# Kernel tuning notes

Measured on AMD Instinct MI355X. Metric: run time of the kernel, lower is better.

The kernel has to match this reference:

```python
import jax, jax.numpy as jnp
import numpy as np

N = 60000    # total nodes
E = 600000   # total edges
R = 7        # num relations (edge types)
D_IN = 64    # raw node feature dim
D = 128      # hidden_channels
D2 = 64      # hidden_channels // 2
L = 2        # num_layers
EPS = 1e-5   # LayerNorm eps (torch default)


def setup_inputs() -> dict:
    key = jax.random.key(0)
    ks = jax.random.split(key, 10)
    s = 0.05  # xavier-ish scale
    return {
        "x": jax.random.normal(ks[0], (N, D_IN), jnp.float32),
        "edge_index": jax.random.randint(ks[1], (2, E), 0, N, dtype=jnp.int64),
        "edge_type": jax.random.randint(ks[2], (E,), 0, R, dtype=jnp.int64),
        "emb_W": jax.random.normal(ks[3], (D_IN, D), jnp.float32) * s,
        "emb_b": jnp.zeros((D,), jnp.float32),
        "rel_W": jax.random.normal(ks[4], (L, R, D, D), jnp.float32) * s,
        "root_W": jax.random.normal(ks[5], (L, D, D), jnp.float32) * s,
        "conv_b": jnp.zeros((L, D), jnp.float32),
        "ln_g": jnp.ones((L, D), jnp.float32),
        "ln_b": jnp.zeros((L, D), jnp.float32),
        "cls_W1": jax.random.normal(ks[6], (D, D2), jnp.float32) * s,
        "cls_b1": jnp.zeros((D2,), jnp.float32),
        "cls_ln_g": jnp.ones((D2,), jnp.float32),
        "cls_ln_b": jnp.zeros((D2,), jnp.float32),
        "cls_W2": jax.random.normal(ks[7], (D2, 1), jnp.float32) * s,
        "cls_b2": jnp.zeros((1,), jnp.float32),
    }


def _layernorm(h, g, b):
    m = h.mean(-1, keepdims=True)
    v = h.var(-1, keepdims=True)  # population variance, matches torch LayerNorm
    return (h - m) * jax.lax.rsqrt(v + EPS) * g + b


def _rgcn_conv(h, Wrel, Wroot, b, src, dst, edge_type):
    # Transform every node by every relation weight: [R*N, D]
    t = jnp.einsum('nd,rde->rne', h, Wrel).reshape(R * N, D)
    msg = t[edge_type * N + src]                      # [E, D] per-edge messages
    seg = edge_type * N + dst                         # per-(relation, dst) segments
    summed = jax.ops.segment_sum(msg, seg, num_segments=R * N)
    cnt = jax.ops.segment_sum(jnp.ones((E,), msg.dtype), seg, num_segments=R * N)
    mean = summed / jnp.maximum(cnt, 1.0)[:, None]    # scatter-mean per relation
    agg = mean.reshape(R, N, D).sum(0)                # sum over relations
    return agg + h @ Wroot + b


def reference(x, edge_index, edge_type, emb_W, emb_b, rel_W, root_W, conv_b,
              ln_g, ln_b, cls_W1, cls_b1, cls_ln_g, cls_ln_b, cls_W2, cls_b2):
    src, dst = edge_index[0], edge_index[1]
    # Node embedding (features clamped as in original forward)
    h = jnp.clip(x, -10.0, 10.0) @ emb_W + emb_b
    for l in range(L):
        h = _rgcn_conv(h, rel_W[l], root_W[l], conv_b[l], src, dst, edge_type)
        h = jax.nn.relu(_layernorm(h, ln_g[l], ln_b[l]))
        # dropout is identity at inference
    # Classifier on transaction nodes (= all nodes in this unified setup)
    z = jax.nn.relu(_layernorm(h @ cls_W1 + cls_b1, cls_ln_g, cls_ln_b))
    return z @ cls_W2 + cls_b2  # [N, 1] logits
```

## Files before the change

### kernel.cpp

```cpp
#include <hip/hip_runtime.h>
#include <hip/hip_bf16.h>

typedef unsigned int uint;
typedef unsigned short ushort;

#define N_NODES 60000
#define N_EDGES 600000
#define NREL 7
#define D_IN 64
#define DHID 128
#define LEPS 1e-5f
#define EMB_BLKS 938

typedef __attribute__((ext_vector_type(8))) short bf16x8v;
typedef __attribute__((ext_vector_type(4))) float f32x4v;

#define AS1C(p) ((const __attribute__((address_space(1))) void*)(p))
#define AS3(p)  ((__attribute__((address_space(3))) void*)(p))

__device__ __forceinline__ float bf2f(uint u16) {
    return __uint_as_float(u16 << 16);
}
__device__ __forceinline__ uint f2bf(float f) {
    uint u = __float_as_uint(f);
    uint lsb = (u >> 16) & 1u;
    u += 0x7fffu + lsb;
    return u >> 16;
}
__device__ __forceinline__ uint pack2(float a, float b) {
    return f2bf(a) | (f2bf(b) << 16);
}

__global__ __launch_bounds__(256) void k_prep(const float* __restrict__ relW,
                                              const float* __restrict__ rootW,
                                              const float* __restrict__ embW,
                                              const int* __restrict__ dst,
                                              const int* __restrict__ et,
                                              ushort* __restrict__ Btr,
                                              ushort* __restrict__ Bte,
                                              int* __restrict__ deg8) {
    __shared__ float t[64][65];
    const int tid = threadIdx.x;
    if (blockIdx.x < 64) {
        const int l  = blockIdx.x >> 5;
        const int b5 = blockIdx.x & 31;
        const int r  = b5 >> 2;
        const int kt = (b5 >> 1) & 1;
        const int jt = b5 & 1;
        #pragma unroll
        for (int i = 0; i < 4; ++i) {
            const int idx = i * 256 + tid;
            const int kr = idx >> 4;
            const int j4 = idx & 15;
            const int kg = kt * 64 + kr;
            const float* src = (r < 7)
                ? (relW + (((size_t)l * 7 + r) * 128 + kg) * 128 + jt * 64 + j4 * 4)
                : (rootW + ((size_t)l * 128 + kg) * 128 + jt * 64 + j4 * 4);
            const float4 v = *(const float4*)src;
            t[kr][j4 * 4 + 0] = v.x; t[kr][j4 * 4 + 1] = v.y;
            t[kr][j4 * 4 + 2] = v.z; t[kr][j4 * 4 + 3] = v.w;
        }
        __syncthreads();
        uint* btd = (uint*)Btr;
        #pragma unroll
        for (int i = 0; i < 8; ++i) {
            const int idx = i * 256 + tid;
            const int jr = idx >> 5;
            const int kd = idx & 31;
            const uint w = pack2(t[kd * 2][jr], t[kd * 2 + 1][jr]);
            btd[((size_t)(l * 8 + r) * 128 + jt * 64 + jr) * 64 + kt * 32 + kd] = w;
        }
    } else if (blockIdx.x < 66) {
        const int jt = blockIdx.x - 64;
        #pragma unroll
        for (int i = 0; i < 4; ++i) {
            const int idx = i * 256 + tid;
            const int kr = idx >> 4;
            const int j4 = idx & 15;
            const float4 v = *(const float4*)(embW + (size_t)kr * 128 + jt * 64 + j4 * 4);
            t[kr][j4 * 4 + 0] = v.x; t[kr][j4 * 4 + 1] = v.y;
            t[kr][j4 * 4 + 2] = v.z; t[kr][j4 * 4 + 3] = v.w;
        }
        __syncthreads();
        uint* btd = (uint*)Bte;
        #pragma unroll
        for (int i = 0; i < 8; ++i) {
            const int idx = i * 256 + tid;
            const int jr = idx >> 5;
            const int kd = idx & 31;
            const uint w = pack2(t[kd * 2][jr], t[kd * 2 + 1][jr]);
            btd[(size_t)(jt * 64 + jr) * 32 + kd] = w;
        }
    } else {
        for (int e = (blockIdx.x - 66) * 256 + tid; e < N_EDGES; e += 1024 * 256)
            atomicAdd(&deg8[dst[e] * 8 + et[e]], 1);
    }
}

__global__ void k_scan1n(const int* __restrict__ deg8, int* __restrict__ rp,
                         int* __restrict__ bsum, int n) {
    __shared__ int s[256];
    const int t = threadIdx.x;
    const int i = blockIdx.x * 256 + t;
    int v = 0;
    if (i < n) {
        const int4 x = *(const int4*)(deg8 + (size_t)i * 8);
        const int4 y = *(const int4*)(deg8 + (size_t)i * 8 + 4);
        v = x.x + x.y + x.z + x.w + y.x + y.y + y.z + y.w;
    }
    s[t] = v;
    __syncthreads();
    for (int o = 1; o < 256; o <<= 1) {
        int uu = (t >= o) ? s[t - o] : 0;
        __syncthreads();
        s[t] += uu;
        __syncthreads();
    }
    if (i < n) rp[i] = s[t] - v;
    if (t == 255) bsum[blockIdx.x] = s[255];
}
__global__ void k_scanmid(int* __restrict__ bs, int nb) {
    __shared__ int s[256];
    __shared__ int carrys;
    const int t = threadIdx.x;
    if (t == 0) carrys = 0;
    __syncthreads();
    const int nch = (nb + 255) / 256;
    for (int ch = 0; ch < nch; ++ch) {
        const int i = ch * 256 + t;
        const int v = (i < nb) ? bs[i] : 0;
        s[t] = v;
        __syncthreads();
        for (int o = 1; o < 256; o <<= 1) {
            int uu = (t >= o) ? s[t - o] : 0;
            __syncthreads();
            s[t] += uu;
            __syncthreads();
        }
        const int carry = carrys;
        if (i < nb) bs[i] = s[t] - v + carry;
        __syncthreads();
        if (t == 255) carrys = carry + s[255];
        __syncthreads();
    }
}
__global__ void k_scanadd(int* __restrict__ a, const int* __restrict__ bsums,
                          int* __restrict__ fill, int n) {
    const int i = blockIdx.x * 256 + threadIdx.x;
    if (i < n) {
        const int v = a[i] + bsums[blockIdx.x];
        a[i] = v;
        fill[i] = v;
    }
    if (blockIdx.x == 0 && threadIdx.x == 0) a[n] = N_EDGES;
}

__global__ __launch_bounds__(256) void k_scatemb(const float* __restrict__ x,
                                                 const ushort* __restrict__ Bte,
                                                 const float* __restrict__ ebias,
                                                 ushort* __restrict__ h,
                                                 const int* __restrict__ src,
                                                 const int* __restrict__ dst,
                                                 const int* __restrict__ et,
                                                 int* __restrict__ fill,
                                                 uint* __restrict__ csr32) {
    __shared__ alignas(16) ushort sa[64 * 64];
    __shared__ alignas(16) ushort sb[128 * 64];
    const int tid = threadIdx.x;
    if (blockIdx.x >= EMB_BLKS) {
        for (int e = (blockIdx.x - EMB_BLKS) * 256 + tid; e < N_EDGES; e += 1024 * 256) {
            const int d = dst[e];
            const int r = et[e];
            const int p = atomicAdd(&fill[d], 1);
            csr32[p] = ((uint)r << 20) | (uint)(r * N_NODES + src[e]);
        }
        return;
    }
    const int lane = tid & 63;
    const int wid = tid >> 6;
    const int wrow = wid >> 1, wcol = wid & 1;
    const int l15 = lane & 15, lh = lane >> 4;
    const int row0 = blockIdx.x * 64;

    #pragma unroll
    for (int i = 0; i < 2; ++i) {
        const int p = i * 256 + tid;
        const int row = p >> 3, gq = p & 7;
        const int n = min(row0 + row, N_NODES - 1);
        const float4 xa = *(const float4*)(x + (size_t)n * 64 + gq * 8);
        const float4 xb = *(const float4*)(x + (size_t)n * 64 + gq * 8 + 4);
        uint w[4];
        w[0] = pack2(fminf(fmaxf(xa.x, -10.f), 10.f), fminf(fmaxf(xa.y, -10.f), 10.f));
        w[1] = pack2(fminf(fmaxf(xa.z, -10.f), 10.f), fminf(fmaxf(xa.w, -10.f), 10.f));
        w[2] = pack2(fminf(fmaxf(xb.x, -10.f), 10.f), fminf(fmaxf(xb.y, -10.f), 10.f));
        w[3] = pack2(fminf(fmaxf(xb.z, -10.f), 10.f), fminf(fmaxf(xb.w, -10.f), 10.f));
        *(uint4*)&sa[(row * 8 + (gq ^ (row & 7))) * 8] = make_uint4(w[0], w[1], w[2], w[3]);
    }
    #pragma unroll
    for (int i = 0; i < 4; ++i) {
        const int p = i * 256 + tid;
        const int row = p >> 3, gq = p & 7;
        const uint4 v = *(const uint4*)((const uint*)Bte + (size_t)row * 32 + gq * 4);
        *(uint4*)&sb[(row * 8 + (gq ^ (row & 7))) * 8] = v;
    }
    float bv[4];
    #pragma unroll
    for (int fn = 0; fn < 4; ++fn) bv[fn] = ebias[wcol * 64 + fn * 16 + l15];
    __syncthreads();

    f32x4v acc[2][4];
    #pragma unroll
    for (int fm = 0; fm < 2; ++fm)
        #pragma unroll
        for (int fn = 0; fn < 4; ++fn)
            acc[fm][fn] = (f32x4v){0.f, 0.f, 0.f, 0.f};
    #pragma unroll
    for (int kh = 0; kh < 2; ++kh) {
        bf16x8v af[2], bfr[4];
        #pragma unroll
        for (int fm = 0; fm < 2; ++fm) {
            const int rowa = wrow * 32 + fm * 16 + l15;
            const int slot = (kh * 4 + lh) ^ (rowa & 7);
            af[fm] = *(const bf16x8v*)&sa[rowa * 64 + slot * 8];
        }
        #pragma unroll
        for (int fn = 0; fn < 4; ++fn) {
            const int rowb = wcol * 64 + fn * 16 + l15;
            const int slot = (kh * 4 + lh) ^ (rowb & 7);
            bfr[fn] = *(const bf16x8v*)&sb[rowb * 64 + slot * 8];
        }
        #pragma unroll
        for (int fm = 0; fm < 2; ++fm)
            #pragma unroll
            for (int fn = 0; fn < 4; ++fn)
                acc[fm][fn] = __builtin_amdgcn_mfma_f32_16x16x32_bf16(
                    af[fm], bfr[fn], acc[fm][fn], 0, 0, 0);
    }
    #pragma unroll
    for (int fm = 0; fm < 2; ++fm)
        #pragma unroll
        for (int r = 0; r < 4; ++r) {
            const int row = row0 + wrow * 32 + fm * 16 + lh * 4 + r;
            if (row < N_NODES) {
                #pragma unroll
                for (int fn = 0; fn < 4; ++fn) {
                    const int col = wcol * 64 + fn * 16 + l15;
                    h[(size_t)row * 128 + col] = (ushort)f2bf(acc[fm][fn][r] + bv[fn]);
                }
            }
        }
}

__global__ __launch_bounds__(512) void k_trans(const ushort* __restrict__ h16,
                                               const ushort* __restrict__ Btr,
                                               ushort* __restrict__ T16,
                                               int nrows) {
    __shared__ alignas(16) ushort sa[2][8192];
    __shared__ alignas(16) ushort sb[2][8192];
    const int tid = threadIdx.x;
    const int lane = tid & 63;
    const int wid = tid >> 6;
    const int wrow = wid >> 1, wcol = wid & 1;
    const int l15 = lane & 15, lh = lane >> 4;
    const int row0 = blockIdx.x * 128;
    const int bj = blockIdx.y;

    int prow[2], pG[2], arow[2];
    #pragma unroll
    for (int hf = 0; hf < 2; ++hf) {
        const int p = hf * 512 + wid * 64 + lane;
        const int r = p >> 3;
        prow[hf] = r;
        pG[hf] = (p & 7) ^ (r & 7);
        arow[hf] = min(row0 + r, nrows - 1);
    }
    #pragma unroll
    for (int kt = 0; kt < 2; ++kt) {
        #pragma unroll
        for (int hf = 0; hf < 2; ++hf) {
            const ushort* ga = h16 + (size_t)arow[hf] * 128 + kt * 64 + pG[hf] * 8;
            __builtin_amdgcn_global_load_lds(AS1C(ga),
                AS3(&sa[kt][(hf * 512 + wid * 64) * 8]), 16, 0, 0);
            const ushort* gb = Btr + ((size_t)bj * 128 + prow[hf]) * 128 + kt * 64 + pG[hf] * 8;
            __builtin_amdgcn_global_load_lds(AS1C(gb),
                AS3(&sb[kt][(hf * 512 + wid * 64) * 8]), 16, 0, 0);
        }
    }
    __syncthreads();

    f32x4v acc[2][4];
    #pragma unroll
    for (int fm = 0; fm < 2; ++fm)
        #pragma unroll
        for (int fn = 0; fn < 4; ++fn)
            acc[fm][fn] = (f32x4v){0.f, 0.f, 0.f, 0.f};

    #pragma unroll
    for (int kt = 0; kt < 2; ++kt)
        #pragma unroll
        for (int kh = 0; kh < 2; ++kh) {
            bf16x8v af[2], bfr[4];
            #pragma unroll
            for (int fm = 0; fm < 2; ++fm) {
                const int rowa = wrow * 32 + fm * 16 + l15;
                const int slot = (kh * 4 + lh) ^ (rowa & 7);
                af[fm] = *(const bf16x8v*)&sa[kt][rowa * 64 + slot * 8];
            }
            #pragma unroll
            for (int fn = 0; fn < 4; ++fn) {
                const int rowb = wcol * 64 + fn * 16 + l15;
                const int slot = (kh * 4 + lh) ^ (rowb & 7);
                bfr[fn] = *(const bf16x8v*)&sb[kt][rowb * 64 + slot * 8];
            }
            #pragma unroll
            for (int fm = 0; fm < 2; ++fm)
                #pragma unroll
                for (int fn = 0; fn < 4; ++fn)
                    acc[fm][fn] = __builtin_amdgcn_mfma_f32_16x16x32_bf16(
                        af[fm], bfr[fn], acc[fm][fn], 0, 0, 0);
        }

    #pragma unroll
    for (int fm = 0; fm < 2; ++fm)
        #pragma unroll
        for (int r = 0; r < 4; ++r) {
            const int row = row0 + wrow * 32 + fm * 16 + lh * 4 + r;
            if (row < nrows) {
                ushort* tp = T16 + ((size_t)bj * N_NODES + row) * 128 + wcol * 64 + l15;
                #pragma unroll
                for (int fn = 0; fn < 4; ++fn)
                    tp[fn * 16] = (ushort)f2bf(acc[fm][fn][r]);
            }
        }
}

__global__ __launch_bounds__(256) void k_gather(const uint* __restrict__ T32,
                                                const int* __restrict__ rp,
                                                const int* __restrict__ deg8,
                                                const uint* __restrict__ csr32,
                                                const float* __restrict__ bias,
                                                const float* __restrict__ g,
                                                const float* __restrict__ bb,
                                                uint* __restrict__ hout) {
    __shared__ float sinv[4][8];
    const int wave = (blockIdx.x * 256 + threadIdx.x) >> 6;
    const int lane = threadIdx.x & 63;
    const int wid = (threadIdx.x >> 6) & 3;
    const int nwaves = gridDim.x * 4;
    const float2 bias2 = *(const float2*)(bias + 2 * lane);
    const float2 g2 = *(const float2*)(g + 2 * lane);
    const float2 b2 = *(const float2*)(bb + 2 * lane);
    #pragma unroll 1
    for (int n0 = wave; n0 < N_NODES; n0 += nwaves) {
        const int n = __builtin_amdgcn_readfirstlane(n0);
        const int beg = __builtin_amdgcn_readfirstlane(rp[n]);
        const int end = __builtin_amdgcn_readfirstlane(rp[n + 1]);
        if (lane < 8) {
            const int c = deg8[(size_t)n * 8 + lane];
            sinv[wid][lane] = 1.0f / (float)max(c, 1);
        }
        float ax = 0.f, ay = 0.f;
        #pragma unroll 1
        for (int e = beg; e < end; e += 8) {
            const int4 c0 = *(const int4*)(csr32 + e);
            const int4 c1 = *(const int4*)(csr32 + e + 4);
            int t[8] = {c0.x, c0.y, c0.z, c0.w, c1.x, c1.y, c1.z, c1.w};
            #pragma unroll
            for (int q = 0; q < 8; ++q) t[q] = __builtin_amdgcn_readfirstlane(t[q]);
            uint v[8];
            #pragma unroll
            for (int q = 0; q < 8; ++q)
                if (e + q < end) v[q] = T32[(size_t)(t[q] & 0xFFFFF) * 64 + lane];
            #pragma unroll
            for (int q = 0; q < 8; ++q)
                if (e + q < end) {
                    const float w = sinv[wid][(t[q] >> 20) & 7];
                    ax += w * __uint_as_float(v[q] << 16);
                    ay += w * __uint_as_float(v[q] & 0xFFFF0000u);
                }
        }
        const uint vr = T32[((size_t)7 * N_NODES + n) * 64 + lane];
        const float c0f = ax + bf2f(vr & 0xFFFFu) + bias2.x;
        const float c1f = ay + bf2f(vr >> 16) + bias2.y;
        float s = c0f + c1f, sq = c0f * c0f + c1f * c1f;
        #pragma unroll
        for (int o = 1; o < 64; o <<= 1) {
            s += __shfl_xor(s, o, 64);
            sq += __shfl_xor(sq, o, 64);
        }
        const float mean = s * (1.f / 128.f);
        const float var = sq * (1.f / 128.f) - mean * mean;
        const float rs = rsqrtf(var + LEPS);
        const float y0 = fmaxf((c0f - mean) * rs * g2.x + b2.x, 0.f);
        const float y1 = fmaxf((c1f - mean) * rs * g2.y + b2.y, 0.f);
        hout[(size_t)n * 64 + lane] = pack2(y0, y1);
    }
}

__global__ __launch_bounds__(256) void k_cls(const ushort* __restrict__ h16,
                                             const float* __restrict__ W1,
                                             const float* __restrict__ b1,
                                             const float* __restrict__ lg,
                                             const float* __restrict__ lb,
                                             const float* __restrict__ W2,
                                             const float* __restrict__ b2,
                                             float* __restrict__ outp, int nrows) {
    __shared__ ushort Bs[16 * 64 * 8];
    const int tid = threadIdx.x;
    #pragma unroll
    for (int i = 0; i < 8; ++i) {
        const int q = i * 256 + tid;
        const int k = q >> 4;
        const int j0 = (q & 15) * 4;
        const float4 w = *(const float4*)(W1 + (size_t)k * 64 + j0);
        const int gg = k >> 3, kp = k & 7;
        const int jx = (gg & 3) << 4;
        Bs[(gg * 64 + ((j0 + 0) ^ jx)) * 8 + kp] = (ushort)f2bf(w.x);
        Bs[(gg * 64 + ((j0 + 1) ^ jx)) * 8 + kp] = (ushort)f2bf(w.y);
        Bs[(gg * 64 + ((j0 + 2) ^ jx)) * 8 + kp] = (ushort)f2bf(w.z);
        Bs[(gg * 64 + ((j0 + 3) ^ jx)) * 8 + kp] = (ushort)f2bf(w.w);
    }
    const int lane = tid & 63, wid = tid >> 6;
    const int l15 = lane & 15, lh = lane >> 4;
    float lgv[4], lbv[4], w2v[4], b1v[4];
    #pragma unroll
    for (int fn = 0; fn < 4; ++fn) {
        const int col = fn * 16 + l15;
        lgv[fn] = lg[col]; lbv[fn] = lb[col]; w2v[fn] = W2[col]; b1v[fn] = b1[col];
    }
    const float b2v = b2[0];
    __syncthreads();

    const int row0 = blockIdx.x * 128;
    f32x4v acc[2][4];
    #pragma unroll
    for (int fm = 0; fm < 2; ++fm)
        #pragma unroll
        for (int fn = 0; fn < 4; ++fn)
            acc[fm][fn] = (f32x4v){0.f, 0.f, 0.f, 0.f};

    #pragma unroll
    for (int kk = 0; kk < 4; ++kk) {
        bf16x8v af[2], bfr[4];
        #pragma unroll
        for (int fm = 0; fm < 2; ++fm) {
            const int row = min(row0 + wid * 32 + fm * 16 + l15, nrows - 1);
            af[fm] = *(const bf16x8v*)(h16 + (size_t)row * 128 + kk * 32 + lh * 8);
        }
        #pragma unroll
        for (int fn = 0; fn < 4; ++fn) {
            const int gg = kk * 4 + lh;
            const int jc = fn * 16 + l15;
            bfr[fn] = *(const bf16x8v*)&Bs[(gg * 64 + (jc ^ ((gg & 3) << 4))) * 8];
        }
        #pragma unroll
        for (int fm = 0; fm < 2; ++fm)
            #pragma unroll
            for (int fn = 0; fn < 4; ++fn)
                acc[fm][fn] = __builtin_amdgcn_mfma_f32_16x16x32_bf16(
                    af[fm], bfr[fn], acc[fm][fn], 0, 0, 0);
    }

    #pragma unroll
    for (int fm = 0; fm < 2; ++fm)
        #pragma unroll
        for (int r = 0; r < 4; ++r) {
            float cv[4];
            float s = 0.f, sq = 0.f;
            #pragma unroll
            for (int fn = 0; fn < 4; ++fn) {
                cv[fn] = acc[fm][fn][r] + b1v[fn];
                s += cv[fn]; sq += cv[fn] * cv[fn];
            }
            s += __shfl_xor(s, 1, 64); sq += __shfl_xor(sq, 1, 64);
            s += __shfl_xor(s, 2, 64); sq += __shfl_xor(sq, 2, 64);
            s += __shfl_xor(s, 4, 64); sq += __shfl_xor(sq, 4, 64);
            s += __shfl_xor(s, 8, 64); sq += __shfl_xor(sq, 8, 64);
            const float mean = s * (1.f / 64.f);
            const float var = sq * (1.f / 64.f) - mean * mean;
            const float rs = rsqrtf(var + LEPS);
            float dot = 0.f;
            #pragma unroll
            for (int fn = 0; fn < 4; ++fn)
                dot += fmaxf((cv[fn] - mean) * rs * lgv[fn] + lbv[fn], 0.f) * w2v[fn];
            dot += __shfl_xor(dot, 1, 64);
            dot += __shfl_xor(dot, 2, 64);
            dot += __shfl_xor(dot, 4, 64);
            dot += __shfl_xor(dot, 8, 64);
            const int row = row0 + wid * 32 + fm * 16 + lh * 4 + r;
            if (l15 == 0 && row < nrows) outp[row] = dot + b2v;
        }
}

extern "C" void kernel_launch(void* const* d_in, const int* in_sizes, int n_in,
                              void* d_out, int out_size, void* d_ws, size_t ws_size,
                              hipStream_t stream) {
    const float* x      = (const float*)d_in[0];
    const int*   eidx   = (const int*)d_in[1];
    const int*   etype  = (const int*)d_in[2];
    const float* emb_W  = (const float*)d_in[3];
    const float* emb_b  = (const float*)d_in[4];
    const float* rel_W  = (const float*)d_in[5];
    const float* root_W = (const float*)d_in[6];
    const float* conv_b = (const float*)d_in[7];
    const float* ln_g   = (const float*)d_in[8];
    const float* ln_b   = (const float*)d_in[9];
    const float* cls_W1 = (const float*)d_in[10];
    const float* cls_b1 = (const float*)d_in[11];
    const float* cls_lg = (const float*)d_in[12];
    const float* cls_lb = (const float*)d_in[13];
    const float* cls_W2 = (const float*)d_in[14];
    const float* cls_b2 = (const float*)d_in[15];

    const int* srcv = eidx;
    const int* dstv = eidx + N_EDGES;

    char* ws = (char*)d_ws;
    size_t off = 0;
    auto alloc = [&](size_t bytes) { void* p = ws + off; off += (bytes + 255) & ~(size_t)255; return p; };
    ushort* h     = (ushort*)alloc((size_t)N_NODES * 128 * 2);
    ushort* T     = (ushort*)alloc((size_t)8 * N_NODES * 128 * 2);
    int*    rp    = (int*)alloc((size_t)(N_NODES + 1) * 4);
    int*    cnts  = (int*)alloc((size_t)(N_NODES * 9) * 4);
    uint*   csr32 = (uint*)alloc((size_t)(N_EDGES + 8) * 4);
    ushort* Btr   = (ushort*)alloc((size_t)2 * 8 * 128 * 128 * 2);
    ushort* Bte   = (ushort*)alloc((size_t)128 * 64 * 2);
    int*    bs    = (int*)alloc(4096);
    int*    deg8  = cnts;
    int*    fill  = cnts + N_NODES * 8;
    (void)ws_size; (void)n_in; (void)in_sizes; (void)out_size;

    const int SB = (N_NODES + 255) / 256;
    const int ROW_BLKS = (N_NODES + 127) / 128;

    hipMemsetAsync(deg8, 0, (size_t)(N_NODES * 8) * 4, stream);
    k_prep<<<66 + 1024, 256, 0, stream>>>(rel_W, root_W, emb_W, dstv, etype,
                                          Btr, Bte, deg8);
    k_scan1n<<<SB, 256, 0, stream>>>(deg8, rp, bs, N_NODES);
    k_scanmid<<<1, 256, 0, stream>>>(bs, SB);
    k_scanadd<<<SB, 256, 0, stream>>>(rp, bs, fill, N_NODES);
    k_scatemb<<<EMB_BLKS + 1024, 256, 0, stream>>>(x, Bte, emb_b, h,
                                                   srcv, dstv, etype, fill, csr32);

    for (int l = 0; l < 2; ++l) {
        k_trans<<<dim3(ROW_BLKS, 8), 512, 0, stream>>>(
            h, Btr + (size_t)l * 131072, T, N_NODES);
        k_gather<<<2048, 256, 0, stream>>>(
            (const uint*)T, rp, deg8, csr32,
            conv_b + l * 128, ln_g + l * 128, ln_b + l * 128,
            (uint*)h);
    }
    k_cls<<<469, 256, 0, stream>>>(h, cls_W1, cls_b1, cls_lg, cls_lb,
                                   cls_W2, cls_b2, (float*)d_out, N_NODES);
}
```

Before: 230.5 us.

## Move CSR edge scatter from embedding kernel into first transform kernel

The atomic edge-scatter that builds the CSR list now runs as extra blocks of the first-layer relation-transform GEMM instead of sharing a launch with the embedding GEMM. The embedding kernel becomes a pure GEMM, and the transform grid is flattened to 1D with the scatter blocks first. The aim is to hide the latency-bound atomic scatter behind the larger transform GEMM rather than the small embedding. In exchange, the scatter blocks use 512 threads and 512 blocks, and they compete for CUs with the transform tiles.

```diff
diff --git a/kernel.cpp b/kernel.cpp
--- a/kernel.cpp
+++ b/kernel.cpp
@@ -11,6 +11,8 @@
 #define DHID 128
 #define LEPS 1e-5f
 #define EMB_BLKS 938
+#define ROW_BLKS 469
+#define SCAT_BLKS 512
 
 typedef __attribute__((ext_vector_type(8))) short bf16x8v;
 typedef __attribute__((ext_vector_type(4))) float f32x4v;
@@ -155,27 +157,13 @@
     if (blockIdx.x == 0 && threadIdx.x == 0) a[n] = N_EDGES;
 }
 
-__global__ __launch_bounds__(256) void k_scatemb(const float* __restrict__ x,
-                                                 const ushort* __restrict__ Bte,
-                                                 const float* __restrict__ ebias,
-                                                 ushort* __restrict__ h,
-                                                 const int* __restrict__ src,
-                                                 const int* __restrict__ dst,
-                                                 const int* __restrict__ et,
-                                                 int* __restrict__ fill,
-                                                 uint* __restrict__ csr32) {
+__global__ __launch_bounds__(256) void k_emb(const float* __restrict__ x,
+                                             const ushort* __restrict__ Bte,
+                                             const float* __restrict__ ebias,
+                                             ushort* __restrict__ h) {
     __shared__ alignas(16) ushort sa[64 * 64];
     __shared__ alignas(16) ushort sb[128 * 64];
     const int tid = threadIdx.x;
-    if (blockIdx.x >= EMB_BLKS) {
-        for (int e = (blockIdx.x - EMB_BLKS) * 256 + tid; e < N_EDGES; e += 1024 * 256) {
-            const int d = dst[e];
-            const int r = et[e];
-            const int p = atomicAdd(&fill[d], 1);
-            csr32[p] = ((uint)r << 20) | (uint)(r * N_NODES + src[e]);
-        }
-        return;
-    }
     const int lane = tid & 63;
     const int wid = tid >> 6;
     const int wrow = wid >> 1, wcol = wid & 1;
@@ -251,19 +239,34 @@
         }
 }
 
-__global__ __launch_bounds__(512) void k_trans(const ushort* __restrict__ h16,
-                                               const ushort* __restrict__ Btr,
-                                               ushort* __restrict__ T16,
-                                               int nrows) {
+__global__ __launch_bounds__(512) void k_transcat(const ushort* __restrict__ h16,
+                                                  const ushort* __restrict__ Btr,
+                                                  ushort* __restrict__ T16,
+                                                  const int* __restrict__ src,
+                                                  const int* __restrict__ dst,
+                                                  const int* __restrict__ et,
+                                                  int* __restrict__ fill,
+                                                  uint* __restrict__ csr32,
+                                                  int nscat) {
     __shared__ alignas(16) ushort sa[2][8192];
     __shared__ alignas(16) ushort sb[2][8192];
     const int tid = threadIdx.x;
+    if (blockIdx.x < nscat) {
+        for (int e = blockIdx.x * 512 + tid; e < N_EDGES; e += SCAT_BLKS * 512) {
+            const int d = dst[e];
+            const int r = et[e];
+            const int p = atomicAdd(&fill[d], 1);
+            csr32[p] = ((uint)r << 20) | (uint)(r * N_NODES + src[e]);
+        }
+        return;
+    }
+    const int lin = blockIdx.x - nscat;
+    const int bj = lin & 7;
+    const int row0 = (lin >> 3) * 128;
     const int lane = tid & 63;
     const int wid = tid >> 6;
     const int wrow = wid >> 1, wcol = wid & 1;
     const int l15 = lane & 15, lh = lane >> 4;
-    const int row0 = blockIdx.x * 128;
-    const int bj = blockIdx.y;
 
     int prow[2], pG[2], arow[2];
     #pragma unroll
@@ -272,7 +275,7 @@
         const int r = p >> 3;
         prow[hf] = r;
         pG[hf] = (p & 7) ^ (r & 7);
-        arow[hf] = min(row0 + r, nrows - 1);
+        arow[hf] = min(row0 + r, N_NODES - 1);
     }
     #pragma unroll
     for (int kt = 0; kt < 2; ++kt) {
@@ -325,7 +328,7 @@
         #pragma unroll
         for (int r = 0; r < 4; ++r) {
             const int row = row0 + wrow * 32 + fm * 16 + lh * 4 + r;
-            if (row < nrows) {
+            if (row < N_NODES) {
                 ushort* tp = T16 + ((size_t)bj * N_NODES + row) * 128 + wcol * 64 + l15;
                 #pragma unroll
                 for (int fn = 0; fn < 4; ++fn)
@@ -531,7 +534,6 @@
     (void)ws_size; (void)n_in; (void)in_sizes; (void)out_size;
 
     const int SB = (N_NODES + 255) / 256;
-    const int ROW_BLKS = (N_NODES + 127) / 128;
 
     hipMemsetAsync(deg8, 0, (size_t)(N_NODES * 8) * 4, stream);
     k_prep<<<66 + 1024, 256, 0, stream>>>(rel_W, root_W, emb_W, dstv, etype,
@@ -539,17 +541,20 @@
     k_scan1n<<<SB, 256, 0, stream>>>(deg8, rp, bs, N_NODES);
     k_scanmid<<<1, 256, 0, stream>>>(bs, SB);
     k_scanadd<<<SB, 256, 0, stream>>>(rp, bs, fill, N_NODES);
-    k_scatemb<<<EMB_BLKS + 1024, 256, 0, stream>>>(x, Bte, emb_b, h,
-                                                   srcv, dstv, etype, fill, csr32);
-
-    for (int l = 0; l < 2; ++l) {
-        k_trans<<<dim3(ROW_BLKS, 8), 512, 0, stream>>>(
-            h, Btr + (size_t)l * 131072, T, N_NODES);
-        k_gather<<<2048, 256, 0, stream>>>(
-            (const uint*)T, rp, deg8, csr32,
-            conv_b + l * 128, ln_g + l * 128, ln_b + l * 128,
-            (uint*)h);
-    }
+    k_emb<<<EMB_BLKS, 256, 0, stream>>>(x, Bte, emb_b, h);
+
+    k_transcat<<<SCAT_BLKS + 8 * ROW_BLKS, 512, 0, stream>>>(
+        h, Btr, T, srcv, dstv, etype, fill, csr32, SCAT_BLKS);
+    k_gather<<<2048, 256, 0, stream>>>(
+        (const uint*)T, rp, deg8, csr32,
+        conv_b, ln_g, ln_b, (uint*)h);
+
+    k_transcat<<<8 * ROW_BLKS, 512, 0, stream>>>(
+        h, Btr + (size_t)131072, T, srcv, dstv, etype, fill, csr32, 0);
+    k_gather<<<2048, 256, 0, stream>>>(
+        (const uint*)T, rp, deg8, csr32,
+        conv_b + 128, ln_g + 128, ln_b + 128, (uint*)h);
+
     k_cls<<<469, 256, 0, stream>>>(h, cls_W1, cls_b1, cls_lg, cls_lb,
                                    cls_W2, cls_b2, (float*)d_out, N_NODES);
 }
```

Result: no change. 226.8 us (-1.6%).
